# Performance work log

Hardware: AMD Instinct MI355X
Metric: run time of the kernel (lower is better)

## Reference

```python
import jax, jax.numpy as jnp
import numpy as np

B, L, S, E, D = 16, 2048, 2048, 64, 64

def setup_inputs() -> dict:
    key = jax.random.key(0)
    k1, k2, k3, k4 = jax.random.split(key, 4)
    queries = jax.random.normal(k1, (B, L, E), dtype=jnp.float32)
    keys = jax.random.normal(k2, (B, S, E), dtype=jnp.float32)
    values = jax.random.normal(k3, (B, S, D), dtype=jnp.float32)
    mlp = jax.random.normal(k4, (L, L), dtype=jnp.float32)  # learned seq-mix matrix
    return {"queries": queries, "keys": keys, "values": values, "mlp": mlp}

def reference(queries, keys, values, mlp):
    # scale = 1/sqrt(E) (self.scale is None)
    E_dim = queries.shape[-1]
    scale = 1.0 / jnp.sqrt(jnp.asarray(E_dim, dtype=queries.dtype))
    # scores: [B, L, S]
    scores = jnp.einsum('ble,bse->bls', queries, keys)
    # dropout omitted (eval mode / attention_dropout=0)
    A = jax.nn.softmax(scale * scores, axis=-1)
    # attention output: [B, L, D]
    V = jnp.einsum('bls,bsd->bld', A, values)
    # learned sequence-mixing: [B, L, D] -> [B, P, D] with P == L
    out = jnp.einsum('bld,pl->bpd', V, mlp)
    return out
```

## Files before the change

kernel.cpp:

```cpp
#include <hip/hip_runtime.h>

#define NB 16
#define NL 2048
#define NS 2048
#define NE 64
#define ND 64

typedef float floatx4 __attribute__((ext_vector_type(4)));
typedef _Float16 half8 __attribute__((ext_vector_type(8)));
typedef __fp16 half2v __attribute__((ext_vector_type(2)));

union H8 { half8 v; half2v h2[4]; };

__device__ __forceinline__ half8 cvt8(floatx4 a, floatx4 b) {
  H8 h;
  h.h2[0] = __builtin_amdgcn_cvt_pkrtz(a[0], a[1]);
  h.h2[1] = __builtin_amdgcn_cvt_pkrtz(a[2], a[3]);
  h.h2[2] = __builtin_amdgcn_cvt_pkrtz(b[0], b[1]);
  h.h2[3] = __builtin_amdgcn_cvt_pkrtz(b[2], b[3]);
  return h.v;
}

__device__ __forceinline__ void async16(void* l, const void* g) {
  __builtin_amdgcn_global_load_lds((__attribute__((address_space(1))) void*)g,
                                   (__attribute__((address_space(3))) void*)l, 16, 0, 0);
}

#define B1_WAIT8  { asm volatile("s_waitcnt vmcnt(8)" ::: "memory"); __builtin_amdgcn_s_barrier(); }
#define B1_WAIT0  { asm volatile("s_waitcnt vmcnt(0)" ::: "memory"); __builtin_amdgcn_s_barrier(); }
#define B2_LGKM   { asm volatile("s_waitcnt lgkmcnt(0)" ::: "memory"); __builtin_amdgcn_s_barrier(); }

__device__ __forceinline__ int kinv(int y) {
  return (y & 0x23) | ((y & 8) << 1) | ((y & 4) << 1) | ((y & 16) >> 2);
}

__global__ __launch_bounds__(256) void prep_k(const float* __restrict__ V,
                                              const float* __restrict__ K,
                                              _Float16* __restrict__ Vt,
                                              _Float16* __restrict__ Kh,
                                              int do_k) {
  __shared__ __align__(16) _Float16 Vl[64][72];
  const int bid = blockIdx.x;
  const int t = threadIdx.x;

  if (bid < 512) {
    const int b = bid >> 5;
    const int s0 = (bid & 31) * 64;
    {
      int sl = t & 63;
      int dg = t >> 6;
      const float* src = V + ((size_t)(b * NS + s0 + sl)) * ND + dg * 16;
      int x = kinv(sl);
      #pragma unroll
      for (int c = 0; c < 4; ++c) {
        floatx4 v = *(const floatx4*)(src + c * 4);
        #pragma unroll
        for (int e = 0; e < 4; ++e) Vl[dg * 16 + c * 4 + e][x] = (_Float16)v[e];
      }
    }
    __syncthreads();
    {
      int d = t & 63;
      int xg = t >> 6;
      int dk = (d & 7) << 3;
      #pragma unroll
      for (int h = 0; h < 2; ++h) {
        int x = xg * 16 + h * 8;
        half8 v = *(const half8*)&Vl[d][x];
        *(half8*)(Vt + ((size_t)(b * ND + d)) * NS + s0 + (x ^ dk)) = v;
      }
    }
  } else {
    if (!do_k) return;
    int c = (bid - 512) * 256 + t;
    int j = c & 7;
    int s = (c >> 3) & (NS - 1);
    int b = c >> 14;
    const float* src = K + ((size_t)(b * NS + s)) * NE + j * 8;
    half8 h = cvt8(*(const floatx4*)src, *(const floatx4*)(src + 4));
    *(half8*)(Kh + ((size_t)(b * NS + s)) * NE + (j ^ (s & 7)) * 8) = h;
  }
}

template<bool KH16>
__global__ __launch_bounds__(256) void attn_k(const float* __restrict__ Q,
                                              const void* __restrict__ Ksrc,
                                              const _Float16* __restrict__ Vtp,
                                              _Float16* __restrict__ Vatt,
                                              const float* __restrict__ Mf,
                                              _Float16* __restrict__ Mh) {
  __shared__ __align__(16) char smem[65536];
  const int tid = threadIdx.x;
  const int wid = tid >> 6, lane = tid & 63;
  const int lr = lane & 15, lg = lane >> 4;
  const int g = wid;
  const int L = blockIdx.y * 32 + blockIdx.x;
  const int b = (L & 7) * 2 + ((L >> 3) & 1);
  const int qx = L >> 4;
  const int qbase = qx * 64;
  const _Float16* Kh = (const _Float16*)Ksrc;
  const float* Kf = (const float*)Ksrc;

  constexpr float SC = 0.18033688f;
  half8 qf[4][2];
  #pragma unroll
  for (int sub = 0; sub < 4; ++sub)
    #pragma unroll
    for (int kk = 0; kk < 2; ++kk) {
      const float* qp = Q + ((size_t)(b * NL + qbase + sub * 16 + lr)) * NE + kk * 32 + lg * 8;
      floatx4 a = *(const floatx4*)qp, c = *(const floatx4*)(qp + 4);
      qf[sub][kk] = cvt8(a * SC, c * SC);
    }

  half8 ones;
  #pragma unroll
  for (int i = 0; i < 8; ++i) ones[i] = (_Float16)1.0f;

  floatx4 oacc[4][4], lacc[4];
  #pragma unroll
  for (int s = 0; s < 4; ++s) {
    lacc[s] = (floatx4){0.f, 0.f, 0.f, 0.f};
    #pragma unroll
    for (int m = 0; m < 4; ++m) oacc[s][m] = (floatx4){0.f, 0.f, 0.f, 0.f};
  }

  int kOff[2][2], vOff[4];
  #pragma unroll
  for (int mt = 0; mt < 2; ++mt)
    #pragma unroll
    for (int kk = 0; kk < 2; ++kk) {
      int row = g * 32 + mt * 16 + lr, col = kk * 32 + lg * 8;
      kOff[mt][kk] = (row * 128 + col * 2) ^ ((row & 7) << 4);
    }
  #pragma unroll
  for (int mt = 0; mt < 4; ++mt) {
    int row = mt * 16 + lr;
    vOff[mt] = row * 256 + (g >> 1) * 128 + (((g & 1) * 64 + lg * 16) ^ ((row & 7) << 4));
  }

  auto stageV = [&](int buf, int s0) {
    #pragma unroll
    for (int i = 0; i < 4; ++i) {
      int co = (wid * 4 + i) * 1024;
      int o = co + lane * 16;
      int row = o >> 8, c16 = (o >> 4) & 15;
      async16(smem + 32768 + buf * 16384 + co,
              Vtp + ((size_t)(b * ND + row)) * NS + s0 + c16 * 8);
    }
  };
  auto stageK = [&](int buf, int s0) {
    if constexpr (KH16) {
      #pragma unroll
      for (int i = 0; i < 4; ++i) {
        int co = (wid * 4 + i) * 1024;
        int o = co + lane * 16;
        int row = o >> 7, c8 = (o >> 4) & 7;
        async16(smem + buf * 16384 + co,
                Kh + ((size_t)(b * NS + s0 + row)) * NE + c8 * 8);
      }
    } else {
      int row = tid >> 1, cg = (tid & 1) * 32;
      const float* kp = Kf + ((size_t)(b * NS + s0 + row)) * NE + cg;
      #pragma unroll
      for (int c = 0; c < 4; ++c) {
        half8 h = cvt8(*(const floatx4*)(kp + c * 8), *(const floatx4*)(kp + c * 8 + 4));
        int col = cg + c * 8;
        *(half8*)(smem + buf * 16384 + ((row * 128 + col * 2) ^ ((row & 7) << 4))) = h;
      }
    }
  };

  stageK(0, 0); stageV(0, 0);
  if constexpr (!KH16) __syncthreads();

  for (int t = 0; t < NS / 128; ++t) {
    int buf = t & 1;
    if (t + 1 < NS / 128) {
      stageK(buf ^ 1, (t + 1) * 128); stageV(buf ^ 1, (t + 1) * 128);
      if constexpr (KH16) B1_WAIT8 else __syncthreads();
    } else {
      if constexpr (KH16) B1_WAIT0
    }

    const char* kb = smem + buf * 16384;
    const char* vb = smem + 32768 + buf * 16384;

    half8 kf[2][2];
    #pragma unroll
    for (int mt = 0; mt < 2; ++mt)
      #pragma unroll
      for (int kk = 0; kk < 2; ++kk)
        kf[mt][kk] = *(const half8*)(kb + kOff[mt][kk]);

    H8 bf[4];
    #pragma unroll
    for (int sub = 0; sub < 4; ++sub) {
      floatx4 sacc[2];
      #pragma unroll
      for (int mt = 0; mt < 2; ++mt) sacc[mt] = (floatx4){0.f, 0.f, 0.f, 0.f};
      __builtin_amdgcn_s_setprio(1);
      #pragma unroll
      for (int kk = 0; kk < 2; ++kk)
        #pragma unroll
        for (int mt = 0; mt < 2; ++mt)
          sacc[mt] = __builtin_amdgcn_mfma_f32_16x16x32_f16(kf[mt][kk], qf[sub][kk], sacc[mt], 0, 0, 0);
      __builtin_amdgcn_s_setprio(0);

      float p00 = __builtin_amdgcn_exp2f(sacc[0][0]);
      float p01 = __builtin_amdgcn_exp2f(sacc[0][1]);
      float p02 = __builtin_amdgcn_exp2f(sacc[0][2]);
      float p03 = __builtin_amdgcn_exp2f(sacc[0][3]);
      float p10 = __builtin_amdgcn_exp2f(sacc[1][0]);
      float p11 = __builtin_amdgcn_exp2f(sacc[1][1]);
      float p12 = __builtin_amdgcn_exp2f(sacc[1][2]);
      float p13 = __builtin_amdgcn_exp2f(sacc[1][3]);
      bf[sub].h2[0] = __builtin_amdgcn_cvt_pkrtz(p00, p01);
      bf[sub].h2[1] = __builtin_amdgcn_cvt_pkrtz(p02, p03);
      bf[sub].h2[2] = __builtin_amdgcn_cvt_pkrtz(p10, p11);
      bf[sub].h2[3] = __builtin_amdgcn_cvt_pkrtz(p12, p13);
    }

    __builtin_amdgcn_s_setprio(1);
    #pragma unroll
    for (int mt = 0; mt < 4; ++mt) {
      half8 vt = *(const half8*)(vb + vOff[mt]);
      #pragma unroll
      for (int sub = 0; sub < 4; ++sub)
        oacc[sub][mt] = __builtin_amdgcn_mfma_f32_16x16x32_f16(vt, bf[sub].v, oacc[sub][mt], 0, 0, 0);
    }
    #pragma unroll
    for (int sub = 0; sub < 4; ++sub)
      lacc[sub] = __builtin_amdgcn_mfma_f32_16x16x32_f16(ones, bf[sub].v, lacc[sub], 0, 0, 0);
    __builtin_amdgcn_s_setprio(0);

    if constexpr (KH16) B2_LGKM else __syncthreads();
  }

  {
    char* red = smem;
    if (g != 0) {
      #pragma unroll
      for (int sub = 0; sub < 4; ++sub)
        #pragma unroll
        for (int mt = 0; mt < 4; ++mt) {
          int idx = sub * 4 + mt;
          *(floatx4*)(red + (g - 1) * 16384 + lane * 256 + ((idx ^ (lane & 15)) * 16)) = oacc[sub][mt];
        }
      if (lg == 0) {
        #pragma unroll
        for (int sub = 0; sub < 4; ++sub)
          *(float*)(red + 49152 + (g - 1) * 256 + lr * 16 + sub * 4) = lacc[sub][0];
      }
    }
    __syncthreads();
    if (g == 0) {
      #pragma unroll
      for (int sub = 0; sub < 4; ++sub) {
        float lt = lacc[sub][0];
        #pragma unroll
        for (int gg = 0; gg < 3; ++gg)
          lt += *(const float*)(red + 49152 + gg * 256 + lr * 16 + sub * 4);
        float inv = __builtin_amdgcn_rcpf(lt);
        int l = qbase + sub * 16 + lr;
        #pragma unroll
        for (int mt = 0; mt < 4; ++mt) {
          floatx4 o = oacc[sub][mt];
          int idx = sub * 4 + mt;
          #pragma unroll
          for (int gg = 0; gg < 3; ++gg)
            o += *(const floatx4*)(red + gg * 16384 + lane * 256 + ((idx ^ (lane & 15)) * 16));
          #pragma unroll
          for (int r = 0; r < 4; ++r) {
            int d = mt * 16 + lg * 4 + r;
            int lsw = (l & ~63) | ((l & 63) ^ ((d & 7) << 3));
            Vatt[((size_t)(b * ND + d)) * NL + lsw] = (_Float16)(o[r] * inv);
          }
        }
      }
    }
  }

  if constexpr (KH16) {
    int mb = blockIdx.y * 32 + blockIdx.x;
    #pragma unroll
    for (int q = 0; q < 4; ++q) {
      int c = mb * 1024 + q * 256 + tid;
      int j = c & 255, p = c >> 8;
      const float* src = Mf + (size_t)p * NL + j * 8;
      half8 h = cvt8(*(const floatx4*)src, *(const floatx4*)(src + 4));
      int jo = (j & ~7) | ((j & 7) ^ (p & 7));
      *(half8*)(Mh + (size_t)p * NL + jo * 8) = h;
    }
  }
}

template<bool A16>
__global__ __launch_bounds__(256) void mix_k(const void* __restrict__ Asrc,
                                             const _Float16* __restrict__ Bsrc,
                                             float* __restrict__ out) {
  __shared__ __align__(16) char smem[65536];
  const int tid = threadIdx.x;
  const int wid = tid >> 6, lane = tid & 63;
  const int lr = lane & 15, lg = lane >> 4;
  const int kh = wid & 1;
  const int mw = wid >> 1;
  const int L = blockIdx.y * 32 + blockIdx.x;
  const int i = L >> 3;
  const int p0 = ((L & 7) * 4 + (i & 3)) * 64;
  const int b = i >> 2;
  const _Float16* Ah = (const _Float16*)Asrc;
  const float* Af = (const float*)Asrc;

  floatx4 acc[2][4];
  #pragma unroll
  for (int mt = 0; mt < 2; ++mt)
    #pragma unroll
    for (int nt = 0; nt < 4; ++nt) acc[mt][nt] = (floatx4){0.f, 0.f, 0.f, 0.f};

  auto stage = [&](int buf, int t) {
    int k0 = kh * (NL / 2) + t * 64;
    if constexpr (A16) {
      #pragma unroll
      for (int i2 = 0; i2 < 4; ++i2) {
        int co = (mw * 4 + i2) * 1024;
        int o = co + lane * 16;
        int row = o >> 7, c8 = (o >> 4) & 7;
        async16(smem + kh * 16384 + buf * 8192 + co,
                Ah + ((size_t)(p0 + row)) * NL + k0 + c8 * 8);
      }
    } else {
      int row = (lane & 31) + mw * 32, cg = (lane >> 5) * 32;
      const float* ap = Af + ((size_t)(p0 + row)) * NL + k0 + cg;
      #pragma unroll
      for (int c = 0; c < 4; ++c) {
        half8 h = cvt8(*(const floatx4*)(ap + c * 8), *(const floatx4*)(ap + c * 8 + 4));
        int col = cg + c * 8;
        *(half8*)(smem + kh * 16384 + buf * 8192 +
                  ((row * 128 + col * 2) ^ ((row & 7) << 4))) = h;
      }
    }
    #pragma unroll
    for (int i2 = 0; i2 < 4; ++i2) {
      int co = (mw * 4 + i2) * 1024;
      int o = co + lane * 16;
      int row = o >> 7, c8 = (o >> 4) & 7;
      async16(smem + 32768 + kh * 16384 + buf * 8192 + co,
              Bsrc + ((size_t)(b * ND + row)) * NL + k0 + c8 * 8);
    }
  };

  stage(0, 0);
  if constexpr (!A16) __syncthreads();

  for (int t = 0; t < 16; ++t) {
    int buf = t & 1;
    if (t + 1 < 16) {
      stage(buf ^ 1, t + 1);
      if constexpr (A16) B1_WAIT8 else __syncthreads();
    } else {
      if constexpr (A16) B1_WAIT0
    }
    const char* ab = smem + kh * 16384 + buf * 8192;
    const char* bb = smem + 32768 + kh * 16384 + buf * 8192;
    #pragma unroll
    for (int kk = 0; kk < 2; ++kk) {
      int col = kk * 32 + lg * 8;
      half8 af[2];
      #pragma unroll
      for (int mt = 0; mt < 2; ++mt) {
        int row = mw * 32 + mt * 16 + lr;
        af[mt] = *(const half8*)(ab + ((row * 128 + col * 2) ^ ((row & 7) << 4)));
      }
      __builtin_amdgcn_s_setprio(1);
      #pragma unroll
      for (int nt = 0; nt < 4; ++nt) {
        int row = nt * 16 + lr;
        half8 bfr = *(const half8*)(bb + ((row * 128 + col * 2) ^ ((row & 7) << 4)));
        #pragma unroll
        for (int mt = 0; mt < 2; ++mt)
          acc[mt][nt] = __builtin_amdgcn_mfma_f32_16x16x32_f16(af[mt], bfr, acc[mt][nt], 0, 0, 0);
      }
      __builtin_amdgcn_s_setprio(0);
    }
    if constexpr (A16) B2_LGKM else __syncthreads();
  }

  if (kh == 1) {
    #pragma unroll
    for (int mt = 0; mt < 2; ++mt)
      #pragma unroll
      for (int nt = 0; nt < 4; ++nt) {
        int idx = mt * 4 + nt;
        *(floatx4*)(smem + mw * 8192 + lane * 128 + ((idx ^ (lane & 7)) * 16)) = acc[mt][nt];
      }
  }
  __syncthreads();
  if (kh == 0) {
    #pragma unroll
    for (int mt = 0; mt < 2; ++mt)
      #pragma unroll
      for (int nt = 0; nt < 4; ++nt) {
        int idx = mt * 4 + nt;
        acc[mt][nt] += *(const floatx4*)(smem + mw * 8192 + lane * 128 + ((idx ^ (lane & 7)) * 16));
        #pragma unroll
        for (int r = 0; r < 4; ++r) {
          int p = p0 + mw * 32 + mt * 16 + lg * 4 + r;
          int d = nt * 16 + lr;
          out[((size_t)(b * NL + p)) * ND + d] = acc[mt][nt][r];
        }
      }
  }
}

extern "C" void kernel_launch(void* const* d_in, const int* in_sizes, int n_in,
                              void* d_out, int out_size, void* d_ws, size_t ws_size,
                              hipStream_t stream) {
  (void)in_sizes; (void)n_in; (void)out_size;
  const float* Q = (const float*)d_in[0];
  const float* K = (const float*)d_in[1];
  const float* V = (const float*)d_in[2];
  const float* M = (const float*)d_in[3];
  float* out = (float*)d_out;

  char* ws = (char*)d_ws;
  _Float16* Vtp  = (_Float16*)ws;
  _Float16* Vatt = (_Float16*)(ws + (4u << 20));
  _Float16* Kh   = (_Float16*)(ws + (8u << 20));
  _Float16* Mh   = (_Float16*)(ws + (12u << 20));
  bool big = ws_size >= (size_t)(20u << 20);

  if (big) {
    prep_k<<<1536, 256, 0, stream>>>(V, K, Vtp, Kh, 1);
    attn_k<true><<<dim3(32, 16), 256, 0, stream>>>(Q, Kh, Vtp, Vatt, M, Mh);
    mix_k<true><<<dim3(32, 16), 256, 0, stream>>>(Mh, Vatt, out);
  } else {
    prep_k<<<512, 256, 0, stream>>>(V, K, Vtp, Kh, 0);
    attn_k<false><<<dim3(32, 16), 256, 0, stream>>>(Q, K, Vtp, Vatt, nullptr, nullptr);
    mix_k<false><<<dim3(32, 16), 256, 0, stream>>>(M, Vatt, out);
  }
}
```

Measured before the change: 56.60 us.

## Share K/V tiles across two query halves per block with triple-buffered staging

The attention kernel now runs 512 threads per block, processing 128 query rows as two 64-row halves that share each staged K/V tile. This halves global K/V staging traffic per query and halves the grid. The K/V pipeline moves from double to triple buffering, dropping the end-of-iteration barrier so only one barrier per tile remains. In exchange the kernel uses about 98KB of LDS per block, which limits occupancy to one block per CU, and the fused M-conversion indexing is remapped to the smaller grid.

```diff
diff --git a/kernel.cpp b/kernel.cpp
--- a/kernel.cpp
+++ b/kernel.cpp
@@ -83,21 +83,22 @@
 }
 
 template<bool KH16>
-__global__ __launch_bounds__(256) void attn_k(const float* __restrict__ Q,
+__global__ __launch_bounds__(512) void attn_k(const float* __restrict__ Q,
                                               const void* __restrict__ Ksrc,
                                               const _Float16* __restrict__ Vtp,
                                               _Float16* __restrict__ Vatt,
                                               const float* __restrict__ Mf,
                                               _Float16* __restrict__ Mh) {
-  __shared__ __align__(16) char smem[65536];
+  __shared__ __align__(16) char smem[100352];
   const int tid = threadIdx.x;
   const int wid = tid >> 6, lane = tid & 63;
   const int lr = lane & 15, lg = lane >> 4;
-  const int g = wid;
-  const int L = blockIdx.y * 32 + blockIdx.x;
+  const int g = wid & 3;
+  const int qh = wid >> 2;
+  const int L = blockIdx.y * 16 + blockIdx.x;
   const int b = (L & 7) * 2 + ((L >> 3) & 1);
   const int qx = L >> 4;
-  const int qbase = qx * 64;
+  const int qbase = qx * 128 + qh * 64;
   const _Float16* Kh = (const _Float16*)Ksrc;
   const float* Kf = (const float*)Ksrc;
 
@@ -140,29 +141,29 @@
 
   auto stageV = [&](int buf, int s0) {
     #pragma unroll
-    for (int i = 0; i < 4; ++i) {
-      int co = (wid * 4 + i) * 1024;
+    for (int i = 0; i < 2; ++i) {
+      int co = (wid * 2 + i) * 1024;
       int o = co + lane * 16;
       int row = o >> 8, c16 = (o >> 4) & 15;
-      async16(smem + 32768 + buf * 16384 + co,
+      async16(smem + 49152 + buf * 16384 + co,
               Vtp + ((size_t)(b * ND + row)) * NS + s0 + c16 * 8);
     }
   };
   auto stageK = [&](int buf, int s0) {
     if constexpr (KH16) {
       #pragma unroll
-      for (int i = 0; i < 4; ++i) {
-        int co = (wid * 4 + i) * 1024;
+      for (int i = 0; i < 2; ++i) {
+        int co = (wid * 2 + i) * 1024;
         int o = co + lane * 16;
         int row = o >> 7, c8 = (o >> 4) & 7;
         async16(smem + buf * 16384 + co,
                 Kh + ((size_t)(b * NS + s0 + row)) * NE + c8 * 8);
       }
     } else {
-      int row = tid >> 1, cg = (tid & 1) * 32;
+      int row = tid >> 2, cg = (tid & 3) * 16;
       const float* kp = Kf + ((size_t)(b * NS + s0 + row)) * NE + cg;
       #pragma unroll
-      for (int c = 0; c < 4; ++c) {
+      for (int c = 0; c < 2; ++c) {
         half8 h = cvt8(*(const floatx4*)(kp + c * 8), *(const floatx4*)(kp + c * 8 + 4));
         int col = cg + c * 8;
         *(half8*)(smem + buf * 16384 + ((row * 128 + col * 2) ^ ((row & 7) << 4))) = h;
@@ -171,19 +172,25 @@
   };
 
   stageK(0, 0); stageV(0, 0);
-  if constexpr (!KH16) __syncthreads();
-
+
+  int br = 0;
   for (int t = 0; t < NS / 128; ++t) {
-    int buf = t & 1;
+    int bn = (br == 2) ? 0 : br + 1;
     if (t + 1 < NS / 128) {
-      stageK(buf ^ 1, (t + 1) * 128); stageV(buf ^ 1, (t + 1) * 128);
-      if constexpr (KH16) B1_WAIT8 else __syncthreads();
+      stageK(bn, (t + 1) * 128); stageV(bn, (t + 1) * 128);
+      if constexpr (KH16) {
+        asm volatile("s_waitcnt vmcnt(4)" ::: "memory");
+        __builtin_amdgcn_s_barrier();
+      } else __syncthreads();
     } else {
-      if constexpr (KH16) B1_WAIT0
-    }
-
-    const char* kb = smem + buf * 16384;
-    const char* vb = smem + 32768 + buf * 16384;
+      if constexpr (KH16) {
+        asm volatile("s_waitcnt vmcnt(0)" ::: "memory");
+        __builtin_amdgcn_s_barrier();
+      } else __syncthreads();
+    }
+
+    const char* kb = smem + br * 16384;
+    const char* vb = smem + 49152 + br * 16384;
 
     half8 kf[2][2];
     #pragma unroll
@@ -232,12 +239,14 @@
     for (int sub = 0; sub < 4; ++sub)
       lacc[sub] = __builtin_amdgcn_mfma_f32_16x16x32_f16(ones, bf[sub].v, lacc[sub], 0, 0, 0);
     __builtin_amdgcn_s_setprio(0);
-
-    if constexpr (KH16) B2_LGKM else __syncthreads();
-  }
+    br = bn;
+  }
+
+  __syncthreads();
 
   {
-    char* red = smem;
+    char* red = smem + qh * 49152;
+    char* lred = smem + 98304 + qh * 768;
     if (g != 0) {
       #pragma unroll
       for (int sub = 0; sub < 4; ++sub)
@@ -249,7 +258,7 @@
       if (lg == 0) {
         #pragma unroll
         for (int sub = 0; sub < 4; ++sub)
-          *(float*)(red + 49152 + (g - 1) * 256 + lr * 16 + sub * 4) = lacc[sub][0];
+          *(float*)(lred + (g - 1) * 256 + lr * 16 + sub * 4) = lacc[sub][0];
       }
     }
     __syncthreads();
@@ -259,7 +268,7 @@
         float lt = lacc[sub][0];
         #pragma unroll
         for (int gg = 0; gg < 3; ++gg)
-          lt += *(const float*)(red + 49152 + gg * 256 + lr * 16 + sub * 4);
+          lt += *(const float*)(lred + gg * 256 + lr * 16 + sub * 4);
         float inv = __builtin_amdgcn_rcpf(lt);
         int l = qbase + sub * 16 + lr;
         #pragma unroll
@@ -281,10 +290,10 @@
   }
 
   if constexpr (KH16) {
-    int mb = blockIdx.y * 32 + blockIdx.x;
+    int mb = blockIdx.y * 16 + blockIdx.x;
     #pragma unroll
     for (int q = 0; q < 4; ++q) {
-      int c = mb * 1024 + q * 256 + tid;
+      int c = mb * 2048 + q * 512 + tid;
       int j = c & 255, p = c >> 8;
       const float* src = Mf + (size_t)p * NL + j * 8;
       half8 h = cvt8(*(const floatx4*)src, *(const floatx4*)(src + 4));
@@ -431,11 +440,11 @@
 
   if (big) {
     prep_k<<<1536, 256, 0, stream>>>(V, K, Vtp, Kh, 1);
-    attn_k<true><<<dim3(32, 16), 256, 0, stream>>>(Q, Kh, Vtp, Vatt, M, Mh);
+    attn_k<true><<<dim3(16, 16), 512, 0, stream>>>(Q, Kh, Vtp, Vatt, M, Mh);
     mix_k<true><<<dim3(32, 16), 256, 0, stream>>>(Mh, Vatt, out);
   } else {
     prep_k<<<512, 256, 0, stream>>>(V, K, Vtp, Kh, 0);
-    attn_k<false><<<dim3(32, 16), 256, 0, stream>>>(Q, K, Vtp, Vatt, nullptr, nullptr);
+    attn_k<false><<<dim3(16, 16), 512, 0, stream>>>(Q, K, Vtp, Vatt, nullptr, nullptr);
     mix_k<false><<<dim3(32, 16), 256, 0, stream>>>(M, Vatt, out);
   }
 }
```

Result: faster. 54.56 us (-3.6%).
